# Kernel optimization log

Hardware: AMD Instinct MI355X
Metric: run time of the kernel (lower is better)

The kernel has to match this reference:

```python
import jax, jax.numpy as jnp
import numpy as np
import math

D_MODEL = 1024
NUM_HEADS = 16
D_K = D_MODEL // NUM_HEADS


def setup_inputs() -> dict:
    key = jax.random.key(0)
    ks = jax.random.split(key, 5)
    scale = 1.0 / math.sqrt(D_MODEL)
    x = jax.random.normal(ks[0], (2, 2048, D_MODEL), dtype=jnp.float32)
    qkv_w = jax.random.uniform(ks[1], (3 * D_MODEL, D_MODEL), jnp.float32, -scale, scale)
    qkv_b = jax.random.uniform(ks[2], (3 * D_MODEL,), jnp.float32, -scale, scale)
    out_w = jax.random.uniform(ks[3], (D_MODEL, D_MODEL), jnp.float32, -scale, scale)
    out_b = jax.random.uniform(ks[4], (D_MODEL,), jnp.float32, -scale, scale)
    return {"x": x, "qkv_w": qkv_w, "qkv_b": qkv_b, "out_w": out_w, "out_b": out_b}


def reference(x, qkv_w, qkv_b, out_w, out_b):
    B, N, D = x.shape
    # fused QKV projection (torch Linear: x @ W.T + b)
    qkv = x @ qkv_w.T + qkv_b                       # (B, N, 3D)
    qkv = qkv.reshape(B, N, 3, NUM_HEADS, D_K)
    qkv = jnp.transpose(qkv, (2, 0, 3, 1, 4))        # (3, B, H, N, d_k)
    q, k, v = qkv[0], qkv[1], qkv[2]
    attn = jnp.einsum('bhnd,bhmd->bhnm', q, k) / math.sqrt(D_K)  # (B,H,N,N)
    attn = jax.nn.softmax(attn, axis=-1)
    out = jnp.einsum('bhnm,bhmd->bhnd', attn, v)     # (B,H,N,d_k)
    out = jnp.transpose(out, (0, 2, 1, 3)).reshape(B, N, D)
    return out @ out_w.T + out_b
```

## Files before the change

kernel.cpp:

```cpp
#include <hip/hip_runtime.h>
#include <hip/hip_bf16.h>


typedef __bf16 bf16x8 __attribute__((ext_vector_type(8)));
typedef __bf16 bf16x4 __attribute__((ext_vector_type(4)));
typedef short short4v __attribute__((ext_vector_type(4)));
typedef float f32x4 __attribute__((ext_vector_type(4)));

#define QSCALE 0.18033688011112042f

__device__ __forceinline__ unsigned short bfbits(float f) {
    union { __bf16 h; unsigned short u; } cv;
    cv.h = (__bf16)f;
    return cv.u;
}

__device__ __forceinline__ float bf2f(unsigned short u) {
    union { unsigned int i; float f; } v;
    v.i = ((unsigned int)u) << 16;
    return v.f;
}

__device__ __forceinline__ f32x4 mfma16(bf16x4 a, bf16x4 b, f32x4 c) {
#if __has_builtin(__builtin_amdgcn_mfma_f32_16x16x16bf16_1k)
    union { bf16x4 h; short4v s; } ua, ub;
    ua.h = a; ub.h = b;
    return __builtin_amdgcn_mfma_f32_16x16x16bf16_1k(ua.s, ub.s, c, 0, 0, 0);
#else
    f32x4 d = c;
    asm volatile("v_mfma_f32_16x16x16_bf16 %0, %1, %2, %0"
                 : "+v"(d) : "v"(a), "v"(b));
    return d;
#endif
}

__device__ __forceinline__ void gl_lds16(const void* g, void* l) {
    __builtin_amdgcn_global_load_lds(
        (__attribute__((address_space(1))) const unsigned int*)g,
        (__attribute__((address_space(3))) unsigned int*)l, 16, 0, 0);
}

__global__ void cvt_all(const float4* __restrict__ x,
                        const float4* __restrict__ wq,
                        const float4* __restrict__ wo,
                        ushort4* __restrict__ d0,
                        ushort4* __restrict__ d1,
                        ushort4* __restrict__ d2) {
    int i = blockIdx.x * blockDim.x + threadIdx.x;
    const int stride = gridDim.x * blockDim.x;
    for (; i < 2097152; i += stride) {
        float4 f;
        ushort4* d;
        int k;
        if (i < 1048576)       { f = x[i];           d = d0; k = i; }
        else if (i < 1835008)  { f = wq[i - 1048576]; d = d1; k = i - 1048576; }
        else                   { f = wo[i - 1835008]; d = d2; k = i - 1835008; }
        ushort4 o;
        o.x = bfbits(f.x); o.y = bfbits(f.y); o.z = bfbits(f.z); o.w = bfbits(f.w);
        d[k] = o;
    }
}

template<int MODE>
__global__ __launch_bounds__(256, 3) void gemm_mfma(
    const unsigned short* __restrict__ A,
    const unsigned short* __restrict__ W,
    const float* __restrict__ bias,
    unsigned short* __restrict__ qo,
    unsigned short* __restrict__ ko,
    unsigned short* __restrict__ vto,
    float* __restrict__ fo) {
    __shared__ __attribute__((aligned(128))) unsigned char smem[32768];
    const int lane = threadIdx.x & 63;
    const int w = threadIdx.x >> 6;
    const int g = lane >> 4, c = lane & 15;
    const int wr = w >> 1, wc = w & 1;
    const int row0 = blockIdx.x * 128;
    const int col0 = blockIdx.y * 128;

    const int rloc = lane >> 3;
    const int csrc = ((lane & 7) ^ rloc) * 8;

    f32x4 acc[4][4] = {};

    for (int kt = 0; kt < 1024; kt += 64) {
        #pragma unroll
        for (int i = 0; i < 4; ++i) {
            const int r = i * 32 + w * 8 + rloc;
            gl_lds16(A + (size_t)(row0 + r) * 1024 + kt + csrc,
                     smem + i * 4096 + w * 1024);
            gl_lds16(W + (size_t)(col0 + r) * 1024 + kt + csrc,
                     smem + 16384 + i * 4096 + w * 1024);
        }
        __syncthreads();

        #pragma unroll
        for (int ks = 0; ks < 2; ++ks) {
            bf16x8 a[4], b[4];
            #pragma unroll
            for (int mi = 0; mi < 4; ++mi) {
                const int r = wr * 64 + mi * 16 + c;
                a[mi] = *(const bf16x8*)(smem + r * 128 + (((ks * 4 + g) ^ (r & 7)) * 16));
            }
            #pragma unroll
            for (int ni = 0; ni < 4; ++ni) {
                const int r = wc * 64 + ni * 16 + c;
                b[ni] = *(const bf16x8*)(smem + 16384 + r * 128 + (((ks * 4 + g) ^ (r & 7)) * 16));
            }
            #pragma unroll
            for (int mi = 0; mi < 4; ++mi)
                #pragma unroll
                for (int ni = 0; ni < 4; ++ni)
                    acc[mi][ni] = __builtin_amdgcn_mfma_f32_16x16x32_bf16(
                        a[mi], b[ni], acc[mi][ni], 0, 0, 0);
        }
        __syncthreads();
    }

    #pragma unroll
    for (int mi = 0; mi < 4; ++mi) {
        #pragma unroll
        for (int ni = 0; ni < 4; ++ni) {
            const int col = col0 + wc * 64 + ni * 16 + c;
            const float bv = bias[col];
            #pragma unroll
            for (int j = 0; j < 4; ++j) {
                const int row = row0 + wr * 64 + mi * 16 + 4 * g + j;
                float v = acc[mi][ni][j] + bv;
                if (MODE == 1) {
                    fo[(size_t)row * 1024 + col] = v;
                } else {
                    const int sec = col >> 10;
                    const int d = col & 1023;
                    const int h = d >> 6, dk = d & 63;
                    const int b_ = row >> 11, n = row & 2047;
                    const int bh = b_ * 16 + h;
                    if (sec == 0)
                        qo[((size_t)(bh * 2048 + n) << 6) + dk] = bfbits(v * QSCALE);
                    else if (sec == 1)
                        ko[((size_t)(bh * 2048 + n) << 6) + dk] = bfbits(v);
                    else
                        vto[(size_t)(bh * 64 + dk) * 2048 + n] = bfbits(v);
                }
            }
        }
    }
}

__global__ __launch_bounds__(256, 4) void attn_flash(
    const unsigned short* __restrict__ Q,
    const unsigned short* __restrict__ K,
    const unsigned short* __restrict__ Vt,
    unsigned short* __restrict__ Pout,
    float* __restrict__ Mb,
    float* __restrict__ Lb) {
    __shared__ __attribute__((aligned(128))) unsigned char smem[32768];
    const int lane = threadIdx.x & 63;
    const int w = threadIdx.x >> 6;
    const int g = lane >> 4, c = lane & 15;
    const int c7 = c & 7;
    const int bh = blockIdx.y;
    const int hz = blockIdx.z;
    const int q0 = blockIdx.x * 128 + w * 32;
    const unsigned short* Qb = Q + (size_t)bh * 2048 * 64;
    const unsigned short* Kb = K + (size_t)bh * 2048 * 64;
    const unsigned short* Vb = Vt + (size_t)bh * 64 * 2048;

    const int rloc = lane >> 3;
    const int csrc = ((lane & 7) ^ (rloc & 7)) * 8;

    const int chunkKV0 = ((0 + g) ^ c7) * 16;
    const int chunkKV1 = ((4 + g) ^ c7) * 16;
    const int ghalf = g >> 1;
    const int gsub = (g & 1) * 8;

    bf16x8 aq[2][2];
    #pragma unroll
    for (int qg = 0; qg < 2; ++qg)
        #pragma unroll
        for (int ks = 0; ks < 2; ++ks)
            aq[qg][ks] = *(const bf16x8*)(Qb + (size_t)(q0 + qg * 16 + c) * 64 + ks * 32 + 8 * g);

    f32x4 oa[4] = {}, ob[4] = {};
    f32x4 la = {}, lb = {};
    float ma = -1e30f, mb = -1e30f;

    bf16x4 ones4;
    #pragma unroll
    for (int i = 0; i < 4; ++i) ones4[i] = (__bf16)1.0f;

    const int gt0 = hz * 16;

    #pragma unroll
    for (int tt = 0; tt < 2; ++tt) {
        const int t = 2 * w + tt;
        const int row = 8 * t + rloc;
        gl_lds16(Kb + (size_t)(gt0 * 64 + row) * 64 + csrc, smem + t * 1024);
        gl_lds16(Vb + (size_t)row * 2048 + gt0 * 64 + csrc, smem + 16384 + t * 1024);
    }
    __syncthreads();

    for (int t = 0; t < 16; ++t) {
        const int cur = t & 1;
        if (t + 1 < 16) {
            const int nb = cur ^ 1;
            const int gt = gt0 + t + 1;
            #pragma unroll
            for (int tt = 0; tt < 2; ++tt) {
                const int ti = 2 * w + tt;
                const int row = 8 * ti + rloc;
                gl_lds16(Kb + (size_t)(gt * 64 + row) * 64 + csrc,
                         smem + nb * 8192 + ti * 1024);
                gl_lds16(Vb + (size_t)row * 2048 + gt * 64 + csrc,
                         smem + 16384 + nb * 8192 + ti * 1024);
            }
        }

        const unsigned char* Kt = smem + cur * 8192;
        const unsigned char* Vtb = smem + 16384 + cur * 8192;

        f32x4 sa[4] = {}, sb[4] = {};
        __builtin_amdgcn_s_setprio(1);
        #pragma unroll
        for (int nj = 0; nj < 4; ++nj) {
            bf16x8 bk0 = *(const bf16x8*)(Kt + nj * 2048 + c * 128 + chunkKV0);
            bf16x8 bk1 = *(const bf16x8*)(Kt + nj * 2048 + c * 128 + chunkKV1);
            sa[nj] = __builtin_amdgcn_mfma_f32_16x16x32_bf16(bk0, aq[0][0], sa[nj], 0, 0, 0);
            sa[nj] = __builtin_amdgcn_mfma_f32_16x16x32_bf16(bk1, aq[0][1], sa[nj], 0, 0, 0);
            sb[nj] = __builtin_amdgcn_mfma_f32_16x16x32_bf16(bk0, aq[1][0], sb[nj], 0, 0, 0);
            sb[nj] = __builtin_amdgcn_mfma_f32_16x16x32_bf16(bk1, aq[1][1], sb[nj], 0, 0, 0);
        }
        __builtin_amdgcn_s_setprio(0);

        float pa = sa[0][0], pb = sb[0][0];
        #pragma unroll
        for (int nj = 0; nj < 4; ++nj)
            #pragma unroll
            for (int j = 0; j < 4; ++j) {
                pa = fmaxf(pa, sa[nj][j]);
                pb = fmaxf(pb, sb[nj][j]);
            }

        const bool trig = (pa > ma + 8.f) || (pb > mb + 8.f);
        if (__any((int)trig)) {
            float rm = pa;
            rm = fmaxf(rm, __shfl_xor(rm, 16));
            rm = fmaxf(rm, __shfl_xor(rm, 32));
            float mnew = fmaxf(ma, rm);
            float sc = __builtin_amdgcn_exp2f(ma - mnew);
            ma = mnew;
            #pragma unroll
            for (int j = 0; j < 4; ++j) {
                const float scj = __shfl(sc, 4 * g + j);
                la[j] *= scj;
                #pragma unroll
                for (int ni = 0; ni < 4; ++ni) oa[ni][j] *= scj;
            }
            rm = pb;
            rm = fmaxf(rm, __shfl_xor(rm, 16));
            rm = fmaxf(rm, __shfl_xor(rm, 32));
            mnew = fmaxf(mb, rm);
            sc = __builtin_amdgcn_exp2f(mb - mnew);
            mb = mnew;
            #pragma unroll
            for (int j = 0; j < 4; ++j) {
                const float scj = __shfl(sc, 4 * g + j);
                lb[j] *= scj;
                #pragma unroll
                for (int ni = 0; ni < 4; ++ni) ob[ni][j] *= scj;
            }
        }

        bf16x4 qa_[4], qb_[4];
        #pragma unroll
        for (int nj = 0; nj < 4; ++nj)
            #pragma unroll
            for (int j = 0; j < 4; ++j) {
                qa_[nj][j] = (__bf16)__builtin_amdgcn_exp2f(sa[nj][j] - ma);
                qb_[nj][j] = (__bf16)__builtin_amdgcn_exp2f(sb[nj][j] - mb);
            }

        f32x4 lta = {}, ltb = {};
        __builtin_amdgcn_s_setprio(1);
        #pragma unroll
        for (int nj = 0; nj < 4; ++nj) {
            lta = mfma16(qa_[nj], ones4, lta);
            ltb = mfma16(qb_[nj], ones4, ltb);
            #pragma unroll
            for (int ni = 0; ni < 4; ++ni) {
                bf16x4 bv = *(const bf16x4*)(Vtb + (ni * 16 + c) * 128 +
                                             (((2 * nj + ghalf) ^ c7) * 16) + gsub);
                oa[ni] = mfma16(qa_[nj], bv, oa[ni]);
                ob[ni] = mfma16(qb_[nj], bv, ob[ni]);
            }
        }
        __builtin_amdgcn_s_setprio(0);
        la += lta;
        lb += ltb;

        __syncthreads();
    }

    const int b_ = bh >> 4, h = bh & 15;
    unsigned short* Pp = Pout + (size_t)hz * 4194304;
    #pragma unroll
    for (int ni = 0; ni < 4; ++ni) {
        #pragma unroll
        for (int j = 0; j < 4; ++j) {
            const int col = h * 64 + ni * 16 + c;
            const int rowa = b_ * 2048 + q0 + 4 * g + j;
            Pp[(size_t)rowa * 1024 + col] = bfbits(oa[ni][j] / la[j]);
            Pp[(size_t)(rowa + 16) * 1024 + col] = bfbits(ob[ni][j] / lb[j]);
        }
    }
    const int mlbase = (hz * 32 + bh) * 2048 + q0;
    if (g == 0) {
        Mb[mlbase + c] = ma;
        Mb[mlbase + 16 + c] = mb;
    }
    if (c == 0) {
        #pragma unroll
        for (int j = 0; j < 4; ++j) {
            Lb[mlbase + 4 * g + j] = la[j];
            Lb[mlbase + 16 + 4 * g + j] = lb[j];
        }
    }
}

__global__ __launch_bounds__(256) void attn_merge(const float* __restrict__ Mb,
                                                  const float* __restrict__ Lb,
                                                  unsigned short* __restrict__ P) {
    const unsigned tid = blockIdx.x * 256 + threadIdx.x;
    const unsigned base = tid * 8;
    const int r = base >> 10, col = base & 1023;
    const int bh = ((r >> 11) << 4) + (col >> 6);
    const int i0 = bh * 2048 + (r & 2047);
    const float m0 = Mb[i0], m1 = Mb[65536 + i0];
    const float l0 = Lb[i0], l1 = Lb[65536 + i0];
    const float mx = fmaxf(m0, m1);
    float w0 = l0 * __builtin_amdgcn_exp2f(m0 - mx);
    float w1 = l1 * __builtin_amdgcn_exp2f(m1 - mx);
    const float inv = 1.f / (w0 + w1);
    w0 *= inv; w1 *= inv;
    ushort4* p0 = (ushort4*)(P + (size_t)r * 1024 + col);
    const ushort4* p1 = (const ushort4*)(P + 4194304 + (size_t)r * 1024 + col);
    #pragma unroll
    for (int k = 0; k < 2; ++k) {
        ushort4 a = p0[k], b = p1[k], o;
        o.x = bfbits(w0 * bf2f(a.x) + w1 * bf2f(b.x));
        o.y = bfbits(w0 * bf2f(a.y) + w1 * bf2f(b.y));
        o.z = bfbits(w0 * bf2f(a.z) + w1 * bf2f(b.z));
        o.w = bfbits(w0 * bf2f(a.w) + w1 * bf2f(b.w));
        p0[k] = o;
    }
}

extern "C" void kernel_launch(void* const* d_in, const int* in_sizes, int n_in,
                              void* d_out, int out_size, void* d_ws, size_t ws_size,
                              hipStream_t stream) {
    const float* x     = (const float*)d_in[0];
    const float* qkv_w = (const float*)d_in[1];
    const float* qkv_b = (const float*)d_in[2];
    const float* out_w = (const float*)d_in[3];
    const float* out_b = (const float*)d_in[4];
    float* out = (float*)d_out;

    char* ws = (char*)d_ws;
    unsigned short* xb   = (unsigned short*)(ws);
    unsigned short* wqkv = (unsigned short*)(ws + (8u  << 20));
    unsigned short* qb   = (unsigned short*)(ws + (16u << 20));
    unsigned short* kb   = (unsigned short*)(ws + (24u << 20));
    unsigned short* vtb  = (unsigned short*)(ws + (32u << 20));
    unsigned short* wout = (unsigned short*)(ws + (40u << 20));
    float* Mb = (float*)(ws + (42u << 20));
    float* Lb = (float*)(ws + (42u << 20) + (512u << 10));

    cvt_all<<<2048, 256, 0, stream>>>((const float4*)x, (const float4*)qkv_w,
                                      (const float4*)out_w,
                                      (ushort4*)xb, (ushort4*)wqkv, (ushort4*)wout);

    gemm_mfma<0><<<dim3(32, 24), 256, 0, stream>>>(xb, wqkv, qkv_b, qb, kb, vtb, nullptr);

    unsigned short* part = xb;
    attn_flash<<<dim3(16, 32, 2), 256, 0, stream>>>(qb, kb, vtb, part, Mb, Lb);

    attn_merge<<<2048, 256, 0, stream>>>(Mb, Lb, part);

    gemm_mfma<1><<<dim3(32, 8), 256, 0, stream>>>(part, wout, out_b, nullptr, nullptr, nullptr, out);
}
```

Before: 127.2 us.

## Fuse split-KV merge into flash kernel and switch GEMM to 32x32 MFMA

Removes the separate attn_merge launch. Each flash block now bumps an atomic counter per query tile, and the second block to finish merges both partial outputs using the stored max and sum values. The GEMM moves from 16x16x32 MFMAs to 32x32x16 MFMAs with fewer LDS fragment loads per K step, and the row-max reduction is rewritten as a tree. The price is an extra memset, threadfence ordering on the flag path, and a different output register layout in the GEMM epilogue.

After: 324.2 us. 2.55x slower.

```diff
diff --git a/kernel.cpp b/kernel.cpp
--- a/kernel.cpp
+++ b/kernel.cpp
@@ -6,6 +6,7 @@
 typedef __bf16 bf16x4 __attribute__((ext_vector_type(4)));
 typedef short short4v __attribute__((ext_vector_type(4)));
 typedef float f32x4 __attribute__((ext_vector_type(4)));
+typedef float f32x16 __attribute__((ext_vector_type(16)));
 
 #define QSCALE 0.18033688011112042f
 
@@ -73,7 +74,7 @@
     __shared__ __attribute__((aligned(128))) unsigned char smem[32768];
     const int lane = threadIdx.x & 63;
     const int w = threadIdx.x >> 6;
-    const int g = lane >> 4, c = lane & 15;
+    const int c5 = lane & 31, hi = lane >> 5;
     const int wr = w >> 1, wc = w & 1;
     const int row0 = blockIdx.x * 128;
     const int col0 = blockIdx.y * 128;
@@ -81,7 +82,11 @@
     const int rloc = lane >> 3;
     const int csrc = ((lane & 7) ^ rloc) * 8;
 
-    f32x4 acc[4][4] = {};
+    f32x16 acc[2][2] = {};
+
+    const int ra = wr * 64 + c5;
+    const int rb = wc * 64 + c5;
+    const int swa = ra & 7, swb = rb & 7;
 
     for (int kt = 0; kt < 1024; kt += 64) {
         #pragma unroll
@@ -95,38 +100,31 @@
         __syncthreads();
 
         #pragma unroll
-        for (int ks = 0; ks < 2; ++ks) {
-            bf16x8 a[4], b[4];
-            #pragma unroll
-            for (int mi = 0; mi < 4; ++mi) {
-                const int r = wr * 64 + mi * 16 + c;
-                a[mi] = *(const bf16x8*)(smem + r * 128 + (((ks * 4 + g) ^ (r & 7)) * 16));
-            }
-            #pragma unroll
-            for (int ni = 0; ni < 4; ++ni) {
-                const int r = wc * 64 + ni * 16 + c;
-                b[ni] = *(const bf16x8*)(smem + 16384 + r * 128 + (((ks * 4 + g) ^ (r & 7)) * 16));
-            }
-            #pragma unroll
-            for (int mi = 0; mi < 4; ++mi)
-                #pragma unroll
-                for (int ni = 0; ni < 4; ++ni)
-                    acc[mi][ni] = __builtin_amdgcn_mfma_f32_16x16x32_bf16(
-                        a[mi], b[ni], acc[mi][ni], 0, 0, 0);
+        for (int ks = 0; ks < 4; ++ks) {
+            const int ch_a = ((2 * ks + hi) ^ swa) * 16;
+            const int ch_b = ((2 * ks + hi) ^ swb) * 16;
+            bf16x8 a0 = *(const bf16x8*)(smem + ra * 128 + ch_a);
+            bf16x8 a1 = *(const bf16x8*)(smem + (ra + 32) * 128 + ch_a);
+            bf16x8 b0 = *(const bf16x8*)(smem + 16384 + rb * 128 + ch_b);
+            bf16x8 b1 = *(const bf16x8*)(smem + 16384 + (rb + 32) * 128 + ch_b);
+            acc[0][0] = __builtin_amdgcn_mfma_f32_32x32x16_bf16(a0, b0, acc[0][0], 0, 0, 0);
+            acc[0][1] = __builtin_amdgcn_mfma_f32_32x32x16_bf16(a0, b1, acc[0][1], 0, 0, 0);
+            acc[1][0] = __builtin_amdgcn_mfma_f32_32x32x16_bf16(a1, b0, acc[1][0], 0, 0, 0);
+            acc[1][1] = __builtin_amdgcn_mfma_f32_32x32x16_bf16(a1, b1, acc[1][1], 0, 0, 0);
         }
         __syncthreads();
     }
 
     #pragma unroll
-    for (int mi = 0; mi < 4; ++mi) {
-        #pragma unroll
-        for (int ni = 0; ni < 4; ++ni) {
-            const int col = col0 + wc * 64 + ni * 16 + c;
+    for (int mi = 0; mi < 2; ++mi) {
+        #pragma unroll
+        for (int ni = 0; ni < 2; ++ni) {
+            const int col = col0 + wc * 64 + ni * 32 + c5;
             const float bv = bias[col];
             #pragma unroll
-            for (int j = 0; j < 4; ++j) {
-                const int row = row0 + wr * 64 + mi * 16 + 4 * g + j;
-                float v = acc[mi][ni][j] + bv;
+            for (int r = 0; r < 16; ++r) {
+                const int row = row0 + wr * 64 + mi * 32 + (r & 3) + 8 * (r >> 2) + 4 * hi;
+                float v = acc[mi][ni][r] + bv;
                 if (MODE == 1) {
                     fo[(size_t)row * 1024 + col] = v;
                 } else {
@@ -153,8 +151,10 @@
     const unsigned short* __restrict__ Vt,
     unsigned short* __restrict__ Pout,
     float* __restrict__ Mb,
-    float* __restrict__ Lb) {
+    float* __restrict__ Lb,
+    int* __restrict__ flags) {
     __shared__ __attribute__((aligned(128))) unsigned char smem[32768];
+    __shared__ int wflag;
     const int lane = threadIdx.x & 63;
     const int w = threadIdx.x >> 6;
     const int g = lane >> 4, c = lane & 15;
@@ -232,14 +232,19 @@
         }
         __builtin_amdgcn_s_setprio(0);
 
-        float pa = sa[0][0], pb = sb[0][0];
-        #pragma unroll
-        for (int nj = 0; nj < 4; ++nj)
-            #pragma unroll
-            for (int j = 0; j < 4; ++j) {
-                pa = fmaxf(pa, sa[nj][j]);
-                pb = fmaxf(pb, sb[nj][j]);
-            }
+        float pa, pb;
+        {
+            float a0 = fmaxf(fmaxf(sa[0][0], sa[0][1]), fmaxf(sa[0][2], sa[0][3]));
+            float a1 = fmaxf(fmaxf(sa[1][0], sa[1][1]), fmaxf(sa[1][2], sa[1][3]));
+            float a2 = fmaxf(fmaxf(sa[2][0], sa[2][1]), fmaxf(sa[2][2], sa[2][3]));
+            float a3 = fmaxf(fmaxf(sa[3][0], sa[3][1]), fmaxf(sa[3][2], sa[3][3]));
+            pa = fmaxf(fmaxf(a0, a1), fmaxf(a2, a3));
+            float b0 = fmaxf(fmaxf(sb[0][0], sb[0][1]), fmaxf(sb[0][2], sb[0][3]));
+            float b1 = fmaxf(fmaxf(sb[1][0], sb[1][1]), fmaxf(sb[1][2], sb[1][3]));
+            float b2 = fmaxf(fmaxf(sb[2][0], sb[2][1]), fmaxf(sb[2][2], sb[2][3]));
+            float b3 = fmaxf(fmaxf(sb[3][0], sb[3][1]), fmaxf(sb[3][2], sb[3][3]));
+            pb = fmaxf(fmaxf(b0, b1), fmaxf(b2, b3));
+        }
 
         const bool trig = (pa > ma + 8.f) || (pb > mb + 8.f);
         if (__any((int)trig)) {
@@ -325,33 +330,39 @@
             Lb[mlbase + 16 + 4 * g + j] = lb[j];
         }
     }
-}
-
-__global__ __launch_bounds__(256) void attn_merge(const float* __restrict__ Mb,
-                                                  const float* __restrict__ Lb,
-                                                  unsigned short* __restrict__ P) {
-    const unsigned tid = blockIdx.x * 256 + threadIdx.x;
-    const unsigned base = tid * 8;
-    const int r = base >> 10, col = base & 1023;
-    const int bh = ((r >> 11) << 4) + (col >> 6);
-    const int i0 = bh * 2048 + (r & 2047);
-    const float m0 = Mb[i0], m1 = Mb[65536 + i0];
-    const float l0 = Lb[i0], l1 = Lb[65536 + i0];
-    const float mx = fmaxf(m0, m1);
-    float w0 = l0 * __builtin_amdgcn_exp2f(m0 - mx);
-    float w1 = l1 * __builtin_amdgcn_exp2f(m1 - mx);
-    const float inv = 1.f / (w0 + w1);
-    w0 *= inv; w1 *= inv;
-    ushort4* p0 = (ushort4*)(P + (size_t)r * 1024 + col);
-    const ushort4* p1 = (const ushort4*)(P + 4194304 + (size_t)r * 1024 + col);
-    #pragma unroll
-    for (int k = 0; k < 2; ++k) {
-        ushort4 a = p0[k], b = p1[k], o;
-        o.x = bfbits(w0 * bf2f(a.x) + w1 * bf2f(b.x));
-        o.y = bfbits(w0 * bf2f(a.y) + w1 * bf2f(b.y));
-        o.z = bfbits(w0 * bf2f(a.z) + w1 * bf2f(b.z));
-        o.w = bfbits(w0 * bf2f(a.w) + w1 * bf2f(b.w));
-        p0[k] = o;
+
+    __threadfence();
+    __syncthreads();
+    if (threadIdx.x == 0)
+        wflag = atomicAdd(&flags[blockIdx.x * 32 + bh], 1);
+    __syncthreads();
+    if (wflag == 0) return;
+    __threadfence();
+
+    const int oz = 1 - hz;
+    const unsigned short* Pq = Pout + (size_t)oz * 4194304;
+    const int mlq = (oz * 32 + bh) * 2048 + q0;
+    #pragma unroll
+    for (int qg = 0; qg < 2; ++qg) {
+        #pragma unroll
+        for (int j = 0; j < 4; ++j) {
+            const int rr = qg * 16 + 4 * g + j;
+            const float m_o = Mb[mlbase + rr], l_o = Lb[mlbase + rr];
+            const float m_p = Mb[mlq + rr],    l_p = Lb[mlq + rr];
+            const float mx = fmaxf(m_o, m_p);
+            float w_o = l_o * __builtin_amdgcn_exp2f(m_o - mx);
+            float w_p = l_p * __builtin_amdgcn_exp2f(m_p - mx);
+            const float inv = 1.f / (w_o + w_p);
+            w_o *= inv; w_p *= inv;
+            const size_t rowg = (size_t)(b_ * 2048 + q0 + rr) * 1024 + h * 64;
+            #pragma unroll
+            for (int ni = 0; ni < 4; ++ni) {
+                const int col = ni * 16 + c;
+                const float v_own = bf2f(Pp[rowg + col]);
+                const float v_oth = bf2f(Pq[rowg + col]);
+                Pout[rowg + col] = bfbits(w_o * v_own + w_p * v_oth);
+            }
+        }
     }
 }
 
@@ -374,6 +385,9 @@
     unsigned short* wout = (unsigned short*)(ws + (40u << 20));
     float* Mb = (float*)(ws + (42u << 20));
     float* Lb = (float*)(ws + (42u << 20) + (512u << 10));
+    int* flags = (int*)(ws + (43u << 20));
+
+    hipMemsetAsync(flags, 0, 512 * sizeof(int), stream);
 
     cvt_all<<<2048, 256, 0, stream>>>((const float4*)x, (const float4*)qkv_w,
                                       (const float4*)out_w,
@@ -382,9 +396,7 @@
     gemm_mfma<0><<<dim3(32, 24), 256, 0, stream>>>(xb, wqkv, qkv_b, qb, kb, vtb, nullptr);
 
     unsigned short* part = xb;
-    attn_flash<<<dim3(16, 32, 2), 256, 0, stream>>>(qb, kb, vtb, part, Mb, Lb);
-
-    attn_merge<<<2048, 256, 0, stream>>>(Mb, Lb, part);
+    attn_flash<<<dim3(16, 32, 2), 256, 0, stream>>>(qb, kb, vtb, part, Mb, Lb, flags);
 
     gemm_mfma<1><<<dim3(32, 8), 256, 0, stream>>>(part, wout, out_b, nullptr, nullptr, nullptr, out);
 }
```
